# Optimization experiments

Hardware: AMD Instinct MI355X
Metric: run time of the kernel (lower is better)

Reference implementation:

```python
import jax, jax.numpy as jnp
import numpy as np

KSIZE = 3
RES_SCALE = 0.2
WITH_RESIDUAL = True


def setup_inputs() -> dict:
    key = jax.random.key(0)
    x = jax.random.normal(key, (8, 3, 1024, 1024), dtype=jnp.float32)
    return {"x": x}


def reference(x) -> jnp.ndarray:
    B, C, H, W = x.shape
    k = KSIZE
    p = k // 2
    # zero padding matches F.unfold(padding=k//2)
    xp = jnp.pad(x, ((0, 0), (0, 0), (p, p), (p, p)))
    # [B, C, k*k, H, W] stack of shifted views (k*k = 9, small static loop)
    patches = jnp.stack(
        [xp[:, :, di:di + H, dj:dj + W] for di in range(k) for dj in range(k)],
        axis=2,
    )
    # median of odd-sized window = middle element of sorted values
    med = jnp.sort(patches, axis=2)[:, :, (k * k) // 2]
    if WITH_RESIDUAL:
        return x + RES_SCALE * (med - x)
    return med
```

## Files before the change

kernel.cpp:

```cpp
#include <hip/hip_runtime.h>


typedef float v4f __attribute__((ext_vector_type(4)));
typedef unsigned long long u64;

#define S2(a,b) { float _t=fminf(a,b); (b)=fmaxf(a,b); (a)=_t; }
__device__ __forceinline__ float med3f(float a, float b, float c) {
    return fmaxf(fminf(a, b), fminf(fmaxf(a, b), c));
}

constexpr int W = 1024, H = 1024;
constexpr int RS = 16;
constexpr int P  = 6;

#define LOADX4(dst, p) asm volatile("global_load_dwordx4 %0, %1, off" \
    : "=&v"(dst) : "v"((u64)(p)) : "memory")
#define LOADD(dst, p)  asm volatile("global_load_dword %0, %1, off" \
    : "=&v"(dst) : "v"((u64)(p)) : "memory")
#define WAITV(n) do { asm volatile("s_waitcnt vmcnt(" #n ")" ::: "memory"); \
    __builtin_amdgcn_sched_barrier(0); } while (0)

__global__ __launch_bounds__(256, 6) void median_blur_kernel(
    const float* __restrict__ xin, float* __restrict__ out)
{
    const int tx = threadIdx.x;
    const int x0 = tx << 2;
    const int y0 = (int)blockIdx.x * RS;
    const size_t plane = (size_t)blockIdx.y * (size_t)(H * W);
    const float* base  = xin + plane;
    float*       obase = out + plane;

    const bool lE = (tx == 0), rE = (tx == 255);
    const int  xl = lE ? x0     : x0 - 1;
    const int  xr = rE ? x0 + 3 : x0 + 4;
    const bool topB = (blockIdx.x == 0);
    const bool botB = (blockIdx.x == gridDim.x - 1);

    v4f   cc[P];
    float ll[P], rr[P];

#define ISSUE(k) do {                                                     \
        int _y = y0 - 1 + (k);                                            \
        _y = _y < 0 ? 0 : (_y > H - 1 ? H - 1 : _y);                      \
        const float* _rp = base + ((size_t)_y << 10);                     \
        LOADX4(cc[(k) % P], _rp + x0);                                    \
        LOADD(ll[(k) % P], _rp + xl);                                     \
        LOADD(rr[(k) % P], _rp + xr);                                     \
    } while (0)

    ISSUE(0); ISSUE(1); ISSUE(2); ISSUE(3); ISSUE(4);

#pragma unroll
    for (int i = 0; i < RS; ++i) {
        if (i <= RS - 4) ISSUE(i + 5);

        if      (i == 0)  WAITV(9);
        else if (i == 1)  WAITV(10);
        else if (i == 2)  WAITV(11);
        else if (i == 13) WAITV(9);
        else if (i == 14) WAITV(6);
        else if (i == 15) WAITV(3);
        else              WAITV(12);

        const int sT = i % P, sM = (i + 1) % P, sB = (i + 2) % P;

        float t[6] = { lE ? 0.0f : ll[sT], cc[sT].x, cc[sT].y, cc[sT].z, cc[sT].w, rE ? 0.0f : rr[sT] };
        float m[6] = { lE ? 0.0f : ll[sM], cc[sM].x, cc[sM].y, cc[sM].z, cc[sM].w, rE ? 0.0f : rr[sM] };
        float b[6] = { lE ? 0.0f : ll[sB], cc[sB].x, cc[sB].y, cc[sB].z, cc[sB].w, rE ? 0.0f : rr[sB] };

        if (i == 0) {
            if (topB) {
#pragma unroll
                for (int j = 0; j < 6; ++j) t[j] = 0.0f;
            }
        }
        if (i == RS - 1) {
            if (botB) {
#pragma unroll
                for (int j = 0; j < 6; ++j) b[j] = 0.0f;
            }
        }

        float lo[6], mi[6], hi[6];
#pragma unroll
        for (int j = 0; j < 6; ++j) {
            float a = t[j], c0 = m[j], d = b[j];
            S2(a, c0); S2(c0, d); S2(a, c0);
            lo[j] = a; mi[j] = c0; hi[j] = d;
        }
        v4f o;
#pragma unroll
        for (int j = 0; j < 4; ++j) {
            const float mxlo = fmaxf(lo[j], fmaxf(lo[j + 1], lo[j + 2]));
            const float mnhi = fminf(hi[j], fminf(hi[j + 1], hi[j + 2]));
            const float mdmi = med3f(mi[j], mi[j + 1], mi[j + 2]);
            const float med  = med3f(mxlo, mdmi, mnhi);
            const float xc   = m[j + 1];
            o[j] = xc + 0.2f * (med - xc);
        }
        *reinterpret_cast<v4f*>(obase + ((size_t)(y0 + i) << 10) + x0) = o;
    }
#undef ISSUE
}

extern "C" void kernel_launch(void* const* d_in, const int* in_sizes, int n_in,
                              void* d_out, int out_size, void* d_ws, size_t ws_size,
                              hipStream_t stream) {
    const float* x = (const float*)d_in[0];
    float* out = (float*)d_out;
    const int planes = in_sizes[0] / (H * W);
    dim3 block(256);
    dim3 grid(H / RS, planes);
    median_blur_kernel<<<grid, block, 0, stream>>>(x, out);
}
```

Measured before the change: 175.5 us.

## Compute one output row per block with wave shuffles for horizontal halos

Replaces the 16-row-per-block software-pipelined loop, with its inline-asm loads and manual vmcnt waits, with a one-row-per-block kernel. Each block loads three rows and gets left and right halo pixels via wavefront shuffles, falling back to scalar loads only at wave edges. Occupancy hint rises from 6 to 8. This drops the per-row halo dword loads and the asm scheduling, but each input row is now read by three blocks instead of being reused across the strip, so it relies on cache hits to avoid extra traffic.

```diff
diff --git a/kernel.cpp b/kernel.cpp
--- a/kernel.cpp
+++ b/kernel.cpp
@@ -2,7 +2,6 @@
 
 
 typedef float v4f __attribute__((ext_vector_type(4)));
-typedef unsigned long long u64;
 
 #define S2(a,b) { float _t=fminf(a,b); (b)=fmaxf(a,b); (a)=_t; }
 __device__ __forceinline__ float med3f(float a, float b, float c) {
@@ -10,97 +9,72 @@
 }
 
 constexpr int W = 1024, H = 1024;
-constexpr int RS = 16;
-constexpr int P  = 6;
 
-#define LOADX4(dst, p) asm volatile("global_load_dwordx4 %0, %1, off" \
-    : "=&v"(dst) : "v"((u64)(p)) : "memory")
-#define LOADD(dst, p)  asm volatile("global_load_dword %0, %1, off" \
-    : "=&v"(dst) : "v"((u64)(p)) : "memory")
-#define WAITV(n) do { asm volatile("s_waitcnt vmcnt(" #n ")" ::: "memory"); \
-    __builtin_amdgcn_sched_barrier(0); } while (0)
-
-__global__ __launch_bounds__(256, 6) void median_blur_kernel(
+__global__ __launch_bounds__(256, 8) void median_blur_kernel(
     const float* __restrict__ xin, float* __restrict__ out)
 {
-    const int tx = threadIdx.x;
-    const int x0 = tx << 2;
-    const int y0 = (int)blockIdx.x * RS;
+    const int tx   = threadIdx.x;
+    const int lane = tx & 63;
+    const int x0   = tx << 2;
+    const int y    = (int)blockIdx.x;
     const size_t plane = (size_t)blockIdx.y * (size_t)(H * W);
     const float* base  = xin + plane;
-    float*       obase = out + plane;
 
-    const bool lE = (tx == 0), rE = (tx == 255);
-    const int  xl = lE ? x0     : x0 - 1;
-    const int  xr = rE ? x0 + 3 : x0 + 4;
-    const bool topB = (blockIdx.x == 0);
-    const bool botB = (blockIdx.x == gridDim.x - 1);
+    const int yt = y > 0     ? y - 1 : 0;
+    const int yb = y < H - 1 ? y + 1 : H - 1;
+    const float* rpt = base + ((size_t)yt << 10);
+    const float* rpm = base + ((size_t)y  << 10);
+    const float* rpb = base + ((size_t)yb << 10);
 
-    v4f   cc[P];
-    float ll[P], rr[P];
+    v4f ct = *reinterpret_cast<const v4f*>(rpt + x0);
+    v4f cm = *reinterpret_cast<const v4f*>(rpm + x0);
+    v4f cb = *reinterpret_cast<const v4f*>(rpb + x0);
 
-#define ISSUE(k) do {                                                     \
-        int _y = y0 - 1 + (k);                                            \
-        _y = _y < 0 ? 0 : (_y > H - 1 ? H - 1 : _y);                      \
-        const float* _rp = base + ((size_t)_y << 10);                     \
-        LOADX4(cc[(k) % P], _rp + x0);                                    \
-        LOADD(ll[(k) % P], _rp + xl);                                     \
-        LOADD(rr[(k) % P], _rp + xr);                                     \
-    } while (0)
+    float hlt = __shfl_up(ct.w, 1);
+    float hlm = __shfl_up(cm.w, 1);
+    float hlb = __shfl_up(cb.w, 1);
+    float hrt = __shfl_down(ct.x, 1);
+    float hrm = __shfl_down(cm.x, 1);
+    float hrb = __shfl_down(cb.x, 1);
+    if (lane == 0) {
+        if (tx == 0) { hlt = 0.0f; hlm = 0.0f; hlb = 0.0f; }
+        else         { hlt = rpt[x0 - 1]; hlm = rpm[x0 - 1]; hlb = rpb[x0 - 1]; }
+    }
+    if (lane == 63) {
+        if (tx == 255) { hrt = 0.0f; hrm = 0.0f; hrb = 0.0f; }
+        else           { hrt = rpt[x0 + 4]; hrm = rpm[x0 + 4]; hrb = rpb[x0 + 4]; }
+    }
 
-    ISSUE(0); ISSUE(1); ISSUE(2); ISSUE(3); ISSUE(4);
+    float t[6] = { hlt, ct.x, ct.y, ct.z, ct.w, hrt };
+    float m[6] = { hlm, cm.x, cm.y, cm.z, cm.w, hrm };
+    float b[6] = { hlb, cb.x, cb.y, cb.z, cb.w, hrb };
+    if (y == 0) {
+#pragma unroll
+        for (int j = 0; j < 6; ++j) t[j] = 0.0f;
+    }
+    if (y == H - 1) {
+#pragma unroll
+        for (int j = 0; j < 6; ++j) b[j] = 0.0f;
+    }
 
+    float lo[6], mi[6], hi[6];
 #pragma unroll
-    for (int i = 0; i < RS; ++i) {
-        if (i <= RS - 4) ISSUE(i + 5);
-
-        if      (i == 0)  WAITV(9);
-        else if (i == 1)  WAITV(10);
-        else if (i == 2)  WAITV(11);
-        else if (i == 13) WAITV(9);
-        else if (i == 14) WAITV(6);
-        else if (i == 15) WAITV(3);
-        else              WAITV(12);
-
-        const int sT = i % P, sM = (i + 1) % P, sB = (i + 2) % P;
-
-        float t[6] = { lE ? 0.0f : ll[sT], cc[sT].x, cc[sT].y, cc[sT].z, cc[sT].w, rE ? 0.0f : rr[sT] };
-        float m[6] = { lE ? 0.0f : ll[sM], cc[sM].x, cc[sM].y, cc[sM].z, cc[sM].w, rE ? 0.0f : rr[sM] };
-        float b[6] = { lE ? 0.0f : ll[sB], cc[sB].x, cc[sB].y, cc[sB].z, cc[sB].w, rE ? 0.0f : rr[sB] };
-
-        if (i == 0) {
-            if (topB) {
+    for (int j = 0; j < 6; ++j) {
+        float a = t[j], c0 = m[j], d = b[j];
+        S2(a, c0); S2(c0, d); S2(a, c0);
+        lo[j] = a; mi[j] = c0; hi[j] = d;
+    }
+    v4f o;
 #pragma unroll
-                for (int j = 0; j < 6; ++j) t[j] = 0.0f;
-            }
-        }
-        if (i == RS - 1) {
-            if (botB) {
-#pragma unroll
-                for (int j = 0; j < 6; ++j) b[j] = 0.0f;
-            }
-        }
-
-        float lo[6], mi[6], hi[6];
-#pragma unroll
-        for (int j = 0; j < 6; ++j) {
-            float a = t[j], c0 = m[j], d = b[j];
-            S2(a, c0); S2(c0, d); S2(a, c0);
-            lo[j] = a; mi[j] = c0; hi[j] = d;
-        }
-        v4f o;
-#pragma unroll
-        for (int j = 0; j < 4; ++j) {
-            const float mxlo = fmaxf(lo[j], fmaxf(lo[j + 1], lo[j + 2]));
-            const float mnhi = fminf(hi[j], fminf(hi[j + 1], hi[j + 2]));
-            const float mdmi = med3f(mi[j], mi[j + 1], mi[j + 2]);
-            const float med  = med3f(mxlo, mdmi, mnhi);
-            const float xc   = m[j + 1];
-            o[j] = xc + 0.2f * (med - xc);
-        }
-        *reinterpret_cast<v4f*>(obase + ((size_t)(y0 + i) << 10) + x0) = o;
+    for (int j = 0; j < 4; ++j) {
+        const float mxlo = fmaxf(lo[j], fmaxf(lo[j + 1], lo[j + 2]));
+        const float mnhi = fminf(hi[j], fminf(hi[j + 1], hi[j + 2]));
+        const float mdmi = med3f(mi[j], mi[j + 1], mi[j + 2]);
+        const float med  = med3f(mxlo, mdmi, mnhi);
+        const float xc   = m[j + 1];
+        o[j] = xc + 0.2f * (med - xc);
     }
-#undef ISSUE
+    *reinterpret_cast<v4f*>(out + plane + ((size_t)y << 10) + x0) = o;
 }
 
 extern "C" void kernel_launch(void* const* d_in, const int* in_sizes, int n_in,
@@ -110,6 +84,6 @@
     float* out = (float*)d_out;
     const int planes = in_sizes[0] / (H * W);
     dim3 block(256);
-    dim3 grid(H / RS, planes);
+    dim3 grid(H, planes);
     median_blur_kernel<<<grid, block, 0, stream>>>(x, out);
 }
```

Measured after the change: 177.6 us. No clear change (+1.2%).
